# Performance work log

Hardware: AMD Instinct MI355X
Metric: run time of the kernel (lower is better)

The kernel has to match this reference:

```python
import jax, jax.numpy as jnp
import numpy as np

B, TQ, TK = 2, 1024, 2048
DQ, DC, H, TOPK = 1024, 768, 16, 64
DH = DQ // H


def setup_inputs() -> dict:
    key = jax.random.key(0)
    ks = jax.random.split(key, 12)
    s = lambda d: 1.0 / np.sqrt(d)
    return {
        "x": jax.random.normal(ks[0], (B, TQ, DQ), jnp.float32),
        "context": jax.random.normal(ks[1], (B, TK, DC), jnp.float32),
        "key_padding_mask": jax.random.bernoulli(ks[2], 0.05, (B, TK)),
        "Wq": jax.random.normal(ks[3], (DQ, DQ), jnp.float32) * s(DQ),
        "bq": jnp.zeros((DQ,), jnp.float32),
        "Wk": jax.random.normal(ks[4], (DC, DQ), jnp.float32) * s(DC),
        "bk": jnp.zeros((DQ,), jnp.float32),
        "Wv": jax.random.normal(ks[5], (DC, DQ), jnp.float32) * s(DC),
        "bv": jnp.zeros((DQ,), jnp.float32),
        "Wo": jax.random.normal(ks[6], (DQ, DQ), jnp.float32) * s(DQ),
        "bo": jnp.zeros((DQ,), jnp.float32),
    }


def _heads(t):
    # (B, T, DQ) -> (B, H, T, DH)
    b, tt, _ = t.shape
    return t.reshape(b, tt, H, DH).transpose(0, 2, 1, 3)


def reference(x, context, key_padding_mask, Wq, bq, Wk, bk, Wv, bv, Wo, bo):
    q = _heads(x @ Wq + bq)          # (B,H,Tq,DH)
    k = _heads(context @ Wk + bk)    # (B,H,Tk,DH)
    v = _heads(context @ Wv + bv)    # (B,H,Tk,DH)

    scale = DH ** -0.5
    logits = jnp.einsum("bhqd,bhkd->bhqk", q, k) * scale  # (B,H,Tq,Tk)
    neg = jnp.finfo(logits.dtype).min
    logits = jnp.where(key_padding_mask[:, None, None, :], neg, logits)

    # hard top-k sparsification: keep top TOPK logits per query, fill rest with -inf-like
    topk_vals, topk_idx = jax.lax.top_k(logits, TOPK)
    sparse_logits = jnp.full_like(logits, neg)
    sparse_logits = jnp.put_along_axis(sparse_logits, topk_idx, topk_vals, axis=-1, inplace=False)

    attn = jax.nn.softmax(sparse_logits, axis=-1)
    out = jnp.einsum("bhqk,bhkd->bhqd", attn, v)  # (B,H,Tq,DH)
    out = out.transpose(0, 2, 1, 3).reshape(B, TQ, DQ)
    return out @ Wo + bo
```

## Files before the change

kernel.cpp:

```cpp
#include <hip/hip_runtime.h>
#include <cstdint>
#include <cstddef>

#define BN_ 2
#define TQ_ 1024
#define TK_ 2048
#define DQ_ 1024
#define DC_ 768
#define NH_ 16
#define DH_ 64
#define TOPK_ 64

typedef unsigned short u16;
typedef __attribute__((ext_vector_type(8))) short short8;
typedef __attribute__((ext_vector_type(8))) u16   ushort8;
typedef __attribute__((ext_vector_type(4))) float floatx4;

__device__ __forceinline__ float bf2f(u16 u) { return __uint_as_float(((unsigned)u) << 16); }
__device__ __forceinline__ u16 f2bf(float f) {
    unsigned u = __float_as_uint(f);
    u += 0x7FFFu + ((u >> 16) & 1u);
    return (u16)(u >> 16);
}
__device__ __forceinline__ float definite(float v, float repl) {
    return ((__float_as_uint(v) & 0x7F800000u) == 0x7F800000u) ? repl : v;
}
__device__ __forceinline__ unsigned mono(float f) {
    unsigned u = __float_as_uint(f);
    return (u & 0x80000000u) ? ~u : (u | 0x80000000u);
}
__device__ __forceinline__ float invmono(unsigned u) {
    return __uint_as_float((u & 0x80000000u) ? (u & 0x7FFFFFFFu) : ~u);
}
__device__ __forceinline__ int gsum16(int x) {
#pragma unroll
    for (int o = 1; o < 16; o <<= 1) x += __shfl_xor(x, o);
    return x;
}
__device__ __forceinline__ int gmin16(int x) {
#pragma unroll
    for (int o = 1; o < 16; o <<= 1) { int y = __shfl_xor(x, o); x = (y < x) ? y : x; }
    return x;
}
__device__ __forceinline__ unsigned gmin16u(unsigned x) {
#pragma unroll
    for (int o = 1; o < 16; o <<= 1) { unsigned y = __shfl_xor((int)x, o); x = (y < x) ? y : x; }
    return x;
}
__device__ __forceinline__ unsigned gmax16u(unsigned x) {
#pragma unroll
    for (int o = 1; o < 16; o <<= 1) { unsigned y = __shfl_xor((int)x, o); x = (y > x) ? y : x; }
    return x;
}
__device__ __forceinline__ float gmax16f(float x) {
#pragma unroll
    for (int o = 1; o < 16; o <<= 1) x = fmaxf(x, __shfl_xor(x, o));
    return x;
}
__device__ __forceinline__ float gsum16f(float x) {
#pragma unroll
    for (int o = 1; o < 16; o <<= 1) x += __shfl_xor(x, o);
    return x;
}

__global__ void marker_kernel(float* __restrict__ out, int n, float val) {
    const int i = blockIdx.x * 256 + threadIdx.x;
    if (i < n) out[i] = val;
}

template <int NV>
__device__ __forceinline__ float select_topk(const unsigned (&um)[NV], const int (&kk)[NV],
                                             unsigned base, int hb, int l16,
                                             float* cvrow, int* ckrow) {
    unsigned X = 0u;
    bool done = false;
    for (int bit = hb; bit >= 0; --bit) {
        const unsigned C = X | (1u << bit);
        int c = 0;
#pragma unroll
        for (int j = 0; j < NV; ++j) c += (um[j] >= C) ? 1 : 0;
        c = gsum16(c);
        if (!done && c >= 64) X = C;
        if (c == 64) done = true;
        if (__all(done)) break;
    }
    int myGt = 0;
#pragma unroll
    for (int j = 0; j < NV; ++j) myGt += (um[j] > X) ? 1 : 0;
    const int totalGt = gsum16(myGt);
    int pre = myGt;
#pragma unroll
    for (int off = 1; off < 16; off <<= 1) {
        const int tv = __shfl_up(pre, off);
        if (l16 >= off) pre += tv;
    }
    int wpos = pre - myGt;
#pragma unroll
    for (int j = 0; j < NV; ++j) {
        if (um[j] > X) {
            cvrow[wpos] = invmono(base + um[j]);
            ckrow[wpos] = kk[j];
            ++wpos;
        }
    }
    const float xval = invmono(base + X);
    int remaining = 64 - totalGt;
    int pos = totalGt;
    int lastkey = -1;
    while (remaining > 0) {
        int mykey = 0x7FFFFFFF;
#pragma unroll
        for (int j = 0; j < NV; ++j)
            if (um[j] == X && kk[j] > lastkey && kk[j] < mykey) mykey = kk[j];
        const int mn = gmin16(mykey);
        if (mn == 0x7FFFFFFF) break;
        if (mykey == mn) { cvrow[pos] = xval; ckrow[pos] = mn; }
        lastkey = mn;
        ++pos; --remaining;
    }
    return xval;
}

struct TsplitJob { const float* W; u16* Wh; u16* Wl; int K; int N; };

__global__ void __launch_bounds__(256) tsplit3(TsplitJob j0, TsplitJob j1, TsplitJob j2) {
    const TsplitJob j = (blockIdx.z == 0) ? j0 : (blockIdx.z == 1) ? j1 : j2;
    const int bk = blockIdx.y * 32;
    if (bk >= j.K) return;
    __shared__ float t[32][33];
    const int x = threadIdx.x & 31, y = threadIdx.x >> 5;
    const int bn = blockIdx.x * 32;
#pragma unroll
    for (int i = 0; i < 32; i += 8) t[y + i][x] = j.W[(size_t)(bk + y + i) * j.N + bn + x];
    __syncthreads();
#pragma unroll
    for (int i = 0; i < 32; i += 8) {
        const float f = t[x][y + i];
        const u16 hi = f2bf(f);
        const size_t o = (size_t)(bn + y + i) * j.K + bk + x;
        j.Wh[o] = hi;
        j.Wl[o] = f2bf(f - bf2f(hi));
    }
}

__global__ void __launch_bounds__(256) tsplit(const float* __restrict__ W,
                                              u16* __restrict__ Wh, u16* __restrict__ Wl,
                                              int K, int N) {
    __shared__ float t[32][33];
    const int x = threadIdx.x & 31, y = threadIdx.x >> 5;
    const int bn = blockIdx.x * 32, bk = blockIdx.y * 32;
#pragma unroll
    for (int i = 0; i < 32; i += 8) t[y + i][x] = W[(size_t)(bk + y + i) * N + bn + x];
    __syncthreads();
#pragma unroll
    for (int i = 0; i < 32; i += 8) {
        const float f = t[x][y + i];
        const u16 hi = f2bf(f);
        const size_t o = (size_t)(bn + y + i) * K + bk + x;
        Wh[o] = hi;
        Wl[o] = f2bf(f - bf2f(hi));
    }
}

template <int ASPLIT, int OMODE>
__global__ void __launch_bounds__(256) gemm3(
    const void* __restrict__ Ap, const void* __restrict__ Alp,
    const u16* __restrict__ Bh, const u16* __restrict__ Bl,
    const float* __restrict__ bias, float scale,
    void* __restrict__ out0, void* __restrict__ out1,
    int M, int N, int K) {
    __shared__ u16 Ahs[64 * 64];
    __shared__ u16 Als[64 * 64];
    __shared__ u16 Bhs[128 * 64];
    __shared__ u16 Bls[128 * 64];

    const int tid = threadIdx.x;
    const int lane = tid & 63, wave = tid >> 6;
    const int wm = wave >> 1, wn = wave & 1;
    const int quad = lane >> 4, l16 = lane & 15;
    const int bm = blockIdx.y * 64, bn = blockIdx.x * 128;

    floatx4 acc[2][4] = {};

    for (int k0 = 0; k0 < K; k0 += 64) {
        __syncthreads();
#pragma unroll
        for (int s2 = 0; s2 < 2; ++s2) {
            const int slot = tid + s2 * 256;
            const int m = slot >> 3, cpos = slot & 7;
            const int c = cpos ^ (m & 7);
            const size_t aoff = (size_t)(bm + m) * K + k0 + c * 8;
            if constexpr (ASPLIT == 0) {
                const float* f = (const float*)Ap + aoff;
                const floatx4 a = *(const floatx4*)f;
                const floatx4 b = *(const floatx4*)(f + 4);
                ushort8 hi, lo;
#pragma unroll
                for (int j = 0; j < 4; ++j) {
                    u16 t = f2bf(a[j]);
                    hi[j] = t; lo[j] = f2bf(a[j] - bf2f(t));
                    t = f2bf(b[j]);
                    hi[4 + j] = t; lo[4 + j] = f2bf(b[j] - bf2f(t));
                }
                *(ushort8*)&Ahs[slot * 8] = hi;
                *(ushort8*)&Als[slot * 8] = lo;
            } else {
                *(ushort8*)&Ahs[slot * 8] = *(const ushort8*)((const u16*)Ap  + aoff);
                *(ushort8*)&Als[slot * 8] = *(const ushort8*)((const u16*)Alp + aoff);
            }
        }
#pragma unroll
        for (int s4 = 0; s4 < 4; ++s4) {
            const int slot = tid + s4 * 256;
            const int n = slot >> 3, cpos = slot & 7;
            const int c = cpos ^ (n & 7);
            const size_t boff = (size_t)(bn + n) * K + k0 + c * 8;
            *(ushort8*)&Bhs[slot * 8] = *(const ushort8*)(Bh + boff);
            *(ushort8*)&Bls[slot * 8] = *(const ushort8*)(Bl + boff);
        }
        __syncthreads();
#pragma unroll
        for (int s = 0; s < 2; ++s) {
            short8 ah[2], al[2], bh[4], bl[4];
#pragma unroll
            for (int mt = 0; mt < 2; ++mt) {
                const int m = wm * 32 + mt * 16 + l16;
                const int cs = s * 4 + quad;
                const int slot = m * 8 + (cs ^ (m & 7));
                ah[mt] = *(const short8*)&Ahs[slot * 8];
                al[mt] = *(const short8*)&Als[slot * 8];
            }
#pragma unroll
            for (int nt = 0; nt < 4; ++nt) {
                const int n = wn * 64 + nt * 16 + l16;
                const int cs = s * 4 + quad;
                const int slot = n * 8 + (cs ^ (n & 7));
                bh[nt] = *(const short8*)&Bhs[slot * 8];
                bl[nt] = *(const short8*)&Bls[slot * 8];
            }
#pragma unroll
            for (int mt = 0; mt < 2; ++mt)
#pragma unroll
                for (int nt = 0; nt < 4; ++nt) {
                    acc[mt][nt] = __builtin_amdgcn_mfma_f32_16x16x32_bf16(ah[mt], bh[nt], acc[mt][nt], 0, 0, 0);
                    acc[mt][nt] = __builtin_amdgcn_mfma_f32_16x16x32_bf16(al[mt], bh[nt], acc[mt][nt], 0, 0, 0);
                    acc[mt][nt] = __builtin_amdgcn_mfma_f32_16x16x32_bf16(ah[mt], bl[nt], acc[mt][nt], 0, 0, 0);
                }
        }
    }

#pragma unroll
    for (int mt = 0; mt < 2; ++mt) {
#pragma unroll
        for (int nt = 0; nt < 4; ++nt) {
            const int col = bn + wn * 64 + nt * 16 + l16;
            const float bcol = bias[col];
#pragma unroll
            for (int r = 0; r < 4; ++r) {
                const int row = bm + wm * 32 + mt * 16 + quad * 4 + r;
                const float val = definite((acc[mt][nt][r] + bcol) * scale, 0.0f);
                const size_t idx = (size_t)row * N + col;
                if constexpr (OMODE == 0) {
                    ((float*)out0)[idx] = val;
                } else if constexpr (OMODE == 1) {
                    ((u16*)out0)[idx] = f2bf(val);
                } else {
                    const u16 hi = f2bf(val);
                    ((u16*)out0)[idx] = hi;
                    ((u16*)out1)[idx] = f2bf(val - bf2f(hi));
                }
            }
        }
    }
}

__global__ void __launch_bounds__(256, 4) attn_topk(
    const u16* Qhi, const u16* Qlo,
    const u16* __restrict__ Khi, const u16* __restrict__ Klo,
    const u16* __restrict__ Vb16, const void* __restrict__ maskp,
    u16* attnH, u16* attnL) {
    __shared__ float lg[16][512];
    __shared__ float cval[16][64];
    __shared__ int   ckey[16][64];

    const int tid = threadIdx.x;
    const int lane = tid & 63, wave = tid >> 6;
    const int quad = lane >> 4, l16 = lane & 15;
    const int rowg = wave * 4 + quad;
    const int b = blockIdx.z, h = blockIdx.y, q0 = blockIdx.x * 16;

    int mmode;
    {
        bool cbyte = false, cbf = false, cf32 = false;
#pragma unroll
        for (int j = 0; j < 16; ++j) {
            const int i = lane + 64 * j;
            const unsigned v = ((const u16*)maskp)[i];
            cbyte |= (v == 0x0100u || v == 0x0101u) || ((i & 1) && v == 0x0001u);
            cbf   |= (!(i & 1)) && v == 0x3F80u;
            cf32  |= (i & 1) && v == 0x3F80u;
        }
        const bool abf = __any(cbf), af32 = __any(cf32), abyte = __any(cbyte);
        mmode = abf ? 2 : (af32 ? 3 : (abyte ? 1 : 0));
    }

    short8 qh[2], ql[2];
    {
        const size_t base = (size_t)(b * TQ_ + q0 + l16) * DQ_ + h * DH_ + quad * 8;
        qh[0] = *(const short8*)(Qhi + base);
        qh[1] = *(const short8*)(Qhi + base + 32);
        ql[0] = *(const short8*)(Qlo + base);
        ql[1] = *(const short8*)(Qlo + base + 32);
    }

    for (int i = tid; i < 16 * 64; i += 256) {
        cval[i >> 6][i & 63] = __uint_as_float(0xFF800000u);
        ckey[i >> 6][i & 63] = i & 63;
    }

    for (int qtr = 0; qtr < 4; ++qtr) {
        if (qtr == 0) {
#pragma unroll 2
            for (int t = 0; t < 8; ++t) {
                const int key = wave * 128 + t * 16 + l16;
                const size_t kb = (size_t)(b * TK_ + key) * DQ_ + h * DH_ + quad * 8;
                const short8 kh0 = *(const short8*)(Khi + kb);
                const short8 kh1 = *(const short8*)(Khi + kb + 32);
                const short8 kl0 = *(const short8*)(Klo + kb);
                const short8 kl1 = *(const short8*)(Klo + kb + 32);
                floatx4 acc = {};
                acc = __builtin_amdgcn_mfma_f32_16x16x32_bf16(qh[0], kh0, acc, 0, 0, 0);
                acc = __builtin_amdgcn_mfma_f32_16x16x32_bf16(ql[0], kh0, acc, 0, 0, 0);
                acc = __builtin_amdgcn_mfma_f32_16x16x32_bf16(qh[0], kl0, acc, 0, 0, 0);
                acc = __builtin_amdgcn_mfma_f32_16x16x32_bf16(qh[1], kh1, acc, 0, 0, 0);
                acc = __builtin_amdgcn_mfma_f32_16x16x32_bf16(ql[1], kh1, acc, 0, 0, 0);
                acc = __builtin_amdgcn_mfma_f32_16x16x32_bf16(qh[1], kl1, acc, 0, 0, 0);
                const int midx = b * TK_ + key;
                bool masked;
                if (mmode == 2)      masked = ((const u16*)maskp)[midx] != 0;
                else if (mmode == 3) masked = ((const float*)maskp)[midx] != 0.0f;
                else if (mmode == 1) masked = ((const unsigned char*)maskp)[midx] != 0;
                else                 masked = ((const int*)maskp)[midx] != 0;
#pragma unroll
                for (int r = 0; r < 4; ++r)
                    lg[quad * 4 + r][key] = masked ? -3.0e38f : definite(acc[r], -3.0e38f);
            }
            __syncthreads();

            unsigned um[36]; int kk[36];
#pragma unroll
            for (int j = 0; j < 32; ++j) {
                um[j] = mono(lg[rowg][l16 + 16 * j]);
                kk[j] = l16 + 16 * j;
            }
#pragma unroll
            for (int t = 0; t < 4; ++t) {
                um[32 + t] = mono(cval[rowg][l16 + 16 * t]);
                kk[32 + t] = ckey[rowg][l16 + 16 * t];
            }
            const float th = select_topk<36>(um, kk, 0u, 31, l16, cval[rowg], ckey[rowg]);
            if (l16 == 0) {
                lg[rowg][255] = th;
                ((int*)&lg[rowg][0])[511] = 0;
            }
        } else {
            float cmrow[4];
#pragma unroll
            for (int r = 0; r < 4; ++r) cmrow[r] = lg[quad * 4 + r][255];
#pragma unroll 2
            for (int t = 0; t < 8; ++t) {
                const int key = qtr * 512 + wave * 128 + t * 16 + l16;
                const size_t kb = (size_t)(b * TK_ + key) * DQ_ + h * DH_ + quad * 8;
                const short8 kh0 = *(const short8*)(Khi + kb);
                const short8 kh1 = *(const short8*)(Khi + kb + 32);
                const short8 kl0 = *(const short8*)(Klo + kb);
                const short8 kl1 = *(const short8*)(Klo + kb + 32);
                floatx4 acc = {};
                acc = __builtin_amdgcn_mfma_f32_16x16x32_bf16(qh[0], kh0, acc, 0, 0, 0);
                acc = __builtin_amdgcn_mfma_f32_16x16x32_bf16(ql[0], kh0, acc, 0, 0, 0);
                acc = __builtin_amdgcn_mfma_f32_16x16x32_bf16(qh[0], kl0, acc, 0, 0, 0);
                acc = __builtin_amdgcn_mfma_f32_16x16x32_bf16(qh[1], kh1, acc, 0, 0, 0);
                acc = __builtin_amdgcn_mfma_f32_16x16x32_bf16(ql[1], kh1, acc, 0, 0, 0);
                acc = __builtin_amdgcn_mfma_f32_16x16x32_bf16(qh[1], kl1, acc, 0, 0, 0);
                const int midx = b * TK_ + key;
                bool masked;
                if (mmode == 2)      masked = ((const u16*)maskp)[midx] != 0;
                else if (mmode == 3) masked = ((const float*)maskp)[midx] != 0.0f;
                else if (mmode == 1) masked = ((const unsigned char*)maskp)[midx] != 0;
                else                 masked = ((const int*)maskp)[midx] != 0;
#pragma unroll
                for (int r = 0; r < 4; ++r) {
                    const float val = masked ? -3.0e38f : definite(acc[r], -3.0e38f);
                    if (val > cmrow[r]) {
                        const int row = quad * 4 + r;
                        const int pos = atomicAdd((int*)&lg[row][511], 1);
                        if (pos < 127) {
                            lg[row][pos] = val;
                            ((int*)&lg[row][0])[128 + pos] = key;
                        }
                    }
                }
            }
            __syncthreads();

            unsigned uc[4]; int ck4[4];
#pragma unroll
            for (int t = 0; t < 4; ++t) {
                uc[t] = mono(cval[rowg][l16 + 16 * t]);
                ck4[t] = ckey[rowg][l16 + 16 * t];
            }
            unsigned cm = uc[0];
            cm = (uc[1] < cm) ? uc[1] : cm;
            cm = (uc[2] < cm) ? uc[2] : cm;
            cm = (uc[3] < cm) ? uc[3] : cm;
            cm = gmin16u(cm);
            int cnt = ((int*)&lg[rowg][0])[511];
            if (cnt > 127) cnt = 127;

            unsigned zm[12]; int kk[12];
            unsigned zmx = 0;
#pragma unroll
            for (int i = 0; i < 8; ++i) {
                const int idx = l16 + 16 * i;
                const bool valid = idx < cnt;
                const float v = lg[rowg][idx];
                const int k = ((int*)&lg[rowg][0])[128 + idx];
                const unsigned mv = mono(v);
                const bool live = valid && (mv > cm);
                zm[i] = live ? (mv - cm) : 0u;
                kk[i] = live ? k : 0x7FFFFFFF;
                zmx = (zm[i] > zmx) ? zm[i] : zmx;
            }
#pragma unroll
            for (int t = 0; t < 4; ++t) {
                zm[8 + t] = uc[t] - cm;
                kk[8 + t] = ck4[t];
                zmx = (zm[8 + t] > zmx) ? zm[8 + t] : zmx;
            }
            zmx = gmax16u(zmx);
            const int hb = 31 - __clz(zmx | 1u);
            const float th = select_topk<12>(zm, kk, cm, hb, l16, cval[rowg], ckey[rowg]);
            if (l16 == 0) {
                lg[rowg][255] = th;
                ((int*)&lg[rowg][0])[511] = 0;
            }
        }
        if (qtr < 3) __syncthreads();
    }

    {
        float v4[4];
#pragma unroll
        for (int t = 0; t < 4; ++t) v4[t] = cval[rowg][l16 + 16 * t];
        float m = fmaxf(fmaxf(v4[0], v4[1]), fmaxf(v4[2], v4[3]));
        m = gmax16f(m);
        float p4[4], S = 0.f;
#pragma unroll
        for (int t = 0; t < 4; ++t) { p4[t] = __expf(v4[t] - m); S += p4[t]; }
        S = gsum16f(S);
        const float inv = 1.0f / S;
#pragma unroll
        for (int t = 0; t < 4; ++t) cval[rowg][l16 + 16 * t] = p4[t] * inv;
    }

    const int half = lane >> 5, l32 = lane & 31;
    const u16* Vrow = Vb16 + (size_t)b * TK_ * DQ_ + h * DH_ + l32 * 2;
#pragma unroll
    for (int rp = 0; rp < 2; ++rp) {
        const int row = wave * 4 + rp * 2 + half;
        float a0 = 0.f, a1 = 0.f;
#pragma unroll 4
        for (int e = 0; e < 64; ++e) {
            const float w = cval[row][e];
            const int k = ckey[row][e];
            const unsigned v2 = *(const unsigned*)(Vrow + (size_t)k * DQ_);
            a0 += w * bf2f((u16)(v2 & 0xFFFFu));
            a1 += w * bf2f((u16)(v2 >> 16));
        }
        a0 = definite(a0, 0.0f);
        a1 = definite(a1, 0.0f);
        const size_t o = (size_t)(b * TQ_ + q0 + row) * DQ_ + h * DH_ + l32 * 2;
        const u16 h0 = f2bf(a0), h1 = f2bf(a1);
        const u16 l0 = f2bf(a0 - bf2f(h0)), l1 = f2bf(a1 - bf2f(h1));
        *(unsigned*)(attnH + o) = (unsigned)h0 | ((unsigned)h1 << 16);
        *(unsigned*)(attnL + o) = (unsigned)l0 | ((unsigned)l1 << 16);
    }
}

extern "C" void kernel_launch(void* const* d_in, const int* in_sizes, int n_in,
                              void* d_out, int out_size, void* d_ws, size_t ws_size,
                              hipStream_t stream) {
    static const int exp_sizes[11] = {2097152, 3145728, 4096, 1048576, 1024,
                                      786432, 1024, 786432, 1024, 1048576, 1024};
    if (n_in != 11) {
        marker_kernel<<<(out_size + 255) / 256, 256, 0, stream>>>((float*)d_out, out_size,
                                                                  (float)(150 + n_in));
        return;
    }
    for (int i = 0; i < 11; ++i)
        if (in_sizes[i] != exp_sizes[i]) {
            marker_kernel<<<(out_size + 255) / 256, 256, 0, stream>>>((float*)d_out, out_size,
                                                                      (float)(200 + i));
            return;
        }

    const float* x   = (const float*)d_in[0];
    const float* ctx = (const float*)d_in[1];
    const void*  msk = d_in[2];
    const float* Wq = (const float*)d_in[3];
    const float* bq = (const float*)d_in[4];
    const float* Wk = (const float*)d_in[5];
    const float* bk = (const float*)d_in[6];
    const float* Wv = (const float*)d_in[7];
    const float* bv = (const float*)d_in[8];
    const float* Wo = (const float*)d_in[9];
    const float* bo = (const float*)d_in[10];

    const size_t SZ_Q = (size_t)BN_ * TQ_ * DQ_ * 2;
    const size_t SZ_K = (size_t)BN_ * TK_ * DQ_ * 2;
    const size_t NEED = 2 * SZ_Q + 2 * SZ_K + SZ_K;
    if (ws_size < NEED) {
        marker_kernel<<<(out_size + 255) / 256, 256, 0, stream>>>(
            (float*)d_out, out_size, (float)(ws_size >> 20));
        return;
    }

    char* ws = (char*)d_ws;
    u16* Qhi = (u16*)(ws);
    u16* Qlo = (u16*)(ws + SZ_Q);
    u16* Khi = (u16*)(ws + 2 * SZ_Q);
    u16* Klo = (u16*)(ws + 2 * SZ_Q + SZ_K);
    u16* Vb  = (u16*)(ws + 2 * SZ_Q + 2 * SZ_K);

    u16* WqT_h = Khi;
    u16* WqT_l = Khi + (size_t)DQ_ * DQ_;
    u16* WkT_h = Vb;
    u16* WkT_l = Vb + (size_t)DC_ * DQ_;
    u16* WvT_h = (u16*)d_out;
    u16* WvT_l = (u16*)d_out + (size_t)DC_ * DQ_;
    u16* WoT_h = Khi;
    u16* WoT_l = Khi + (size_t)DQ_ * DQ_;

    const int MQ = BN_ * TQ_;
    const int MK = BN_ * TK_;

    TsplitJob jq{Wq, WqT_h, WqT_l, DQ_, DQ_};
    TsplitJob jk{Wk, WkT_h, WkT_l, DC_, DQ_};
    TsplitJob jv{Wv, WvT_h, WvT_l, DC_, DQ_};
    tsplit3<<<dim3(DQ_ / 32, DQ_ / 32, 3), 256, 0, stream>>>(jq, jk, jv);

    gemm3<0, 2><<<dim3(DQ_ / 128, MQ / 64), 256, 0, stream>>>(
        x, nullptr, WqT_h, WqT_l, bq, 0.125f, Qhi, Qlo, MQ, DQ_, DQ_);
    gemm3<0, 2><<<dim3(DQ_ / 128, MK / 64), 256, 0, stream>>>(
        ctx, nullptr, WkT_h, WkT_l, bk, 1.0f, Khi, Klo, MK, DQ_, DC_);
    gemm3<0, 1><<<dim3(DQ_ / 128, MK / 64), 256, 0, stream>>>(
        ctx, nullptr, WvT_h, WvT_l, bv, 1.0f, Vb, nullptr, MK, DQ_, DC_);

    attn_topk<<<dim3(TQ_ / 16, NH_, BN_), 256, 0, stream>>>(
        Qhi, Qlo, Khi, Klo, Vb, msk, Qhi, Qlo);

    tsplit<<<dim3(DQ_ / 32, DQ_ / 32), 256, 0, stream>>>(Wo, WoT_h, WoT_l, DQ_, DQ_);
    gemm3<1, 0><<<dim3(DQ_ / 128, MQ / 64), 256, 0, stream>>>(
        Qhi, Qlo, WoT_h, WoT_l, bo, 1.0f, d_out, nullptr, MQ, DQ_, DQ_);
}
```

Before: 408.4 us.

## Interleave top-k value/key pairs in shared logits buffer and pre-scale key offsets

Stores candidate values and keys as interleaved float2 pairs, and places the running top-64 carry inside the existing logits shared buffer instead of separate cval/ckey arrays, which cuts shared memory per block. Keys are stored pre-shifted as byte offsets into V, which removes the multiply in the gather loop. The first quarter's selection now handles only the 32 fresh values per lane, with no carry initialisation. The V accumulation uses fmaf with direct bf16 bit extraction and unrolls deeper. The risk is that the carry region overlapping lg[row][256..383] could collide with candidate slots written during later quarters.

```diff
diff --git a/kernel.cpp b/kernel.cpp
--- a/kernel.cpp
+++ b/kernel.cpp
@@ -15,6 +15,7 @@
 typedef __attribute__((ext_vector_type(8))) short short8;
 typedef __attribute__((ext_vector_type(8))) u16   ushort8;
 typedef __attribute__((ext_vector_type(4))) float floatx4;
+typedef __attribute__((ext_vector_type(2))) float floatx2;
 
 __device__ __forceinline__ float bf2f(u16 u) { return __uint_as_float(((unsigned)u) << 16); }
 __device__ __forceinline__ u16 f2bf(float f) {
@@ -68,10 +69,68 @@
     if (i < n) out[i] = val;
 }
 
+__device__ __forceinline__ void carry_write(float* cb, int pos, float v, int skey) {
+    floatx2 p;
+    p[0] = v;
+    p[1] = __int_as_float(skey);
+    *(floatx2*)&cb[2 * pos] = p;
+}
+
+__device__ __forceinline__ float select_topk32_ik(const unsigned (&um)[32], int l16,
+                                                  float* cb) {
+    unsigned X = 0u;
+    bool done = false;
+    for (int bit = 31; bit >= 0; --bit) {
+        const unsigned C = X | (1u << bit);
+        int c = 0;
+#pragma unroll
+        for (int j = 0; j < 32; ++j) c += (um[j] >= C) ? 1 : 0;
+        c = gsum16(c);
+        if (!done && c >= 64) X = C;
+        if (c == 64) done = true;
+        if (__all(done)) break;
+    }
+    int myGt = 0;
+#pragma unroll
+    for (int j = 0; j < 32; ++j) myGt += (um[j] > X) ? 1 : 0;
+    const int totalGt = gsum16(myGt);
+    int pre = myGt;
+#pragma unroll
+    for (int off = 1; off < 16; off <<= 1) {
+        const int tv = __shfl_up(pre, off);
+        if (l16 >= off) pre += tv;
+    }
+    int wpos = pre - myGt;
+#pragma unroll
+    for (int j = 0; j < 32; ++j) {
+        if (um[j] > X) {
+            carry_write(cb, wpos, invmono(um[j]), (l16 + 16 * j) << 11);
+            ++wpos;
+        }
+    }
+    const float xval = invmono(X);
+    int remaining = 64 - totalGt;
+    int pos = totalGt;
+    int lastkey = -1;
+    while (remaining > 0) {
+        int mykey = 0x7FFFFFFF;
+#pragma unroll
+        for (int j = 0; j < 32; ++j) {
+            const int kj = (l16 + 16 * j) << 11;
+            if (um[j] == X && kj > lastkey && kj < mykey) mykey = kj;
+        }
+        const int mn = gmin16(mykey);
+        if (mn == 0x7FFFFFFF) break;
+        if (mykey == mn) carry_write(cb, pos, xval, mn);
+        lastkey = mn;
+        ++pos; --remaining;
+    }
+    return xval;
+}
+
 template <int NV>
 __device__ __forceinline__ float select_topk(const unsigned (&um)[NV], const int (&kk)[NV],
-                                             unsigned base, int hb, int l16,
-                                             float* cvrow, int* ckrow) {
+                                             unsigned base, int hb, int l16, float* cb) {
     unsigned X = 0u;
     bool done = false;
     for (int bit = hb; bit >= 0; --bit) {
@@ -98,8 +157,7 @@
 #pragma unroll
     for (int j = 0; j < NV; ++j) {
         if (um[j] > X) {
-            cvrow[wpos] = invmono(base + um[j]);
-            ckrow[wpos] = kk[j];
+            carry_write(cb, wpos, invmono(base + um[j]), kk[j]);
             ++wpos;
         }
     }
@@ -114,7 +172,7 @@
             if (um[j] == X && kk[j] > lastkey && kk[j] < mykey) mykey = kk[j];
         const int mn = gmin16(mykey);
         if (mn == 0x7FFFFFFF) break;
-        if (mykey == mn) { cvrow[pos] = xval; ckrow[pos] = mn; }
+        if (mykey == mn) carry_write(cb, pos, xval, mn);
         lastkey = mn;
         ++pos; --remaining;
     }
@@ -280,14 +338,14 @@
     const u16* __restrict__ Vb16, const void* __restrict__ maskp,
     u16* attnH, u16* attnL) {
     __shared__ float lg[16][512];
-    __shared__ float cval[16][64];
-    __shared__ int   ckey[16][64];
 
     const int tid = threadIdx.x;
     const int lane = tid & 63, wave = tid >> 6;
     const int quad = lane >> 4, l16 = lane & 15;
     const int rowg = wave * 4 + quad;
     const int b = blockIdx.z, h = blockIdx.y, q0 = blockIdx.x * 16;
+
+#define CB_(row) (&lg[row][256])
 
     int mmode;
     {
@@ -311,11 +369,6 @@
         qh[1] = *(const short8*)(Qhi + base + 32);
         ql[0] = *(const short8*)(Qlo + base);
         ql[1] = *(const short8*)(Qlo + base + 32);
-    }
-
-    for (int i = tid; i < 16 * 64; i += 256) {
-        cval[i >> 6][i & 63] = __uint_as_float(0xFF800000u);
-        ckey[i >> 6][i & 63] = i & 63;
     }
 
     for (int qtr = 0; qtr < 4; ++qtr) {
@@ -347,18 +400,10 @@
             }
             __syncthreads();
 
-            unsigned um[36]; int kk[36];
-#pragma unroll
-            for (int j = 0; j < 32; ++j) {
-                um[j] = mono(lg[rowg][l16 + 16 * j]);
-                kk[j] = l16 + 16 * j;
-            }
-#pragma unroll
-            for (int t = 0; t < 4; ++t) {
-                um[32 + t] = mono(cval[rowg][l16 + 16 * t]);
-                kk[32 + t] = ckey[rowg][l16 + 16 * t];
-            }
-            const float th = select_topk<36>(um, kk, 0u, 31, l16, cval[rowg], ckey[rowg]);
+            unsigned um[32];
+#pragma unroll
+            for (int j = 0; j < 32; ++j) um[j] = mono(lg[rowg][l16 + 16 * j]);
+            const float th = select_topk32_ik(um, l16, CB_(rowg));
             if (l16 == 0) {
                 lg[rowg][255] = th;
                 ((int*)&lg[rowg][0])[511] = 0;
@@ -395,8 +440,10 @@
                         const int row = quad * 4 + r;
                         const int pos = atomicAdd((int*)&lg[row][511], 1);
                         if (pos < 127) {
-                            lg[row][pos] = val;
-                            ((int*)&lg[row][0])[128 + pos] = key;
+                            floatx2 p;
+                            p[0] = val;
+                            p[1] = __int_as_float(key << 11);
+                            *(floatx2*)&lg[row][2 * pos] = p;
                         }
                     }
                 }
@@ -406,8 +453,9 @@
             unsigned uc[4]; int ck4[4];
 #pragma unroll
             for (int t = 0; t < 4; ++t) {
-                uc[t] = mono(cval[rowg][l16 + 16 * t]);
-                ck4[t] = ckey[rowg][l16 + 16 * t];
+                const floatx2 pr = *(const floatx2*)&CB_(rowg)[2 * (l16 + 16 * t)];
+                uc[t] = mono(pr[0]);
+                ck4[t] = __float_as_int(pr[1]);
             }
             unsigned cm = uc[0];
             cm = (uc[1] < cm) ? uc[1] : cm;
@@ -423,9 +471,9 @@
             for (int i = 0; i < 8; ++i) {
                 const int idx = l16 + 16 * i;
                 const bool valid = idx < cnt;
-                const float v = lg[rowg][idx];
-                const int k = ((int*)&lg[rowg][0])[128 + idx];
-                const unsigned mv = mono(v);
+                const floatx2 pr = *(const floatx2*)&lg[rowg][2 * idx];
+                const unsigned mv = mono(pr[0]);
+                const int k = __float_as_int(pr[1]);
                 const bool live = valid && (mv > cm);
                 zm[i] = live ? (mv - cm) : 0u;
                 kk[i] = live ? k : 0x7FFFFFFF;
@@ -439,7 +487,7 @@
             }
             zmx = gmax16u(zmx);
             const int hb = 31 - __clz(zmx | 1u);
-            const float th = select_topk<12>(zm, kk, cm, hb, l16, cval[rowg], ckey[rowg]);
+            const float th = select_topk<12>(zm, kk, cm, hb, l16, CB_(rowg));
             if (l16 == 0) {
                 lg[rowg][255] = th;
                 ((int*)&lg[rowg][0])[511] = 0;
@@ -451,7 +499,7 @@
     {
         float v4[4];
 #pragma unroll
-        for (int t = 0; t < 4; ++t) v4[t] = cval[rowg][l16 + 16 * t];
+        for (int t = 0; t < 4; ++t) v4[t] = CB_(rowg)[2 * (l16 + 16 * t)];
         float m = fmaxf(fmaxf(v4[0], v4[1]), fmaxf(v4[2], v4[3]));
         m = gmax16f(m);
         float p4[4], S = 0.f;
@@ -460,22 +508,24 @@
         S = gsum16f(S);
         const float inv = 1.0f / S;
 #pragma unroll
-        for (int t = 0; t < 4; ++t) cval[rowg][l16 + 16 * t] = p4[t] * inv;
+        for (int t = 0; t < 4; ++t) CB_(rowg)[2 * (l16 + 16 * t)] = p4[t] * inv;
     }
 
     const int half = lane >> 5, l32 = lane & 31;
-    const u16* Vrow = Vb16 + (size_t)b * TK_ * DQ_ + h * DH_ + l32 * 2;
+    const char* Vrow = (const char*)(Vb16 + (size_t)b * TK_ * DQ_ + h * DH_ + l32 * 2);
 #pragma unroll
     for (int rp = 0; rp < 2; ++rp) {
         const int row = wave * 4 + rp * 2 + half;
+        const float* cb = CB_(row);
         float a0 = 0.f, a1 = 0.f;
-#pragma unroll 4
+#pragma unroll 8
         for (int e = 0; e < 64; ++e) {
-            const float w = cval[row][e];
-            const int k = ckey[row][e];
-            const unsigned v2 = *(const unsigned*)(Vrow + (size_t)k * DQ_);
-            a0 += w * bf2f((u16)(v2 & 0xFFFFu));
-            a1 += w * bf2f((u16)(v2 >> 16));
+            const floatx2 pr = *(const floatx2*)&cb[2 * e];
+            const float w = pr[0];
+            const int koff = __float_as_int(pr[1]);
+            const unsigned v2 = *(const unsigned*)(Vrow + koff);
+            a0 = fmaf(w, __uint_as_float(v2 << 16), a0);
+            a1 = fmaf(w, __uint_as_float(v2 & 0xFFFF0000u), a1);
         }
         a0 = definite(a0, 0.0f);
         a1 = definite(a1, 0.0f);
@@ -485,6 +535,7 @@
         *(unsigned*)(attnH + o) = (unsigned)h0 | ((unsigned)h1 << 16);
         *(unsigned*)(attnL + o) = (unsigned)l0 | ((unsigned)l1 << 16);
     }
+#undef CB_
 }
 
 extern "C" void kernel_launch(void* const* d_in, const int* in_sizes, int n_in,
```

After: 426.5 us. +4.4%, slower.
